# Optimization experiments

Hardware: AMD Instinct MI355X
Metric: run time of the kernel (lower is better)

## Reference

```python
import jax, jax.numpy as jnp
import numpy as np
import math

B, T, E, H, L, V = 256, 256, 64, 8, 6, 65
HS = E // H  # head_size = 8


def _pos_encoding():
    position = jnp.arange(T, dtype=jnp.float32)[:, None]
    div_term = jnp.exp(jnp.arange(0, E, 2, dtype=jnp.float32) * (-(math.log(10000.0) / E)))
    pe = jnp.zeros((T, E), dtype=jnp.float32)
    pe = pe.at[:, 0::2].set(jnp.sin(position * div_term))
    pe = pe.at[:, 1::2].set(jnp.cos(position * div_term))
    return pe


def _layernorm(x, g, b, eps=1e-5):
    mu = jnp.mean(x, axis=-1, keepdims=True)
    var = jnp.var(x, axis=-1, keepdims=True)
    return (x - mu) * jax.lax.rsqrt(var + eps) * g + b


def setup_inputs() -> dict:
    key = jax.random.key(0)
    ks = jax.random.split(key, 20)
    s = 0.02
    return {
        "inputs": jax.random.randint(ks[0], (B, T), 0, V),
        "labels": jax.random.randint(ks[1], (B, T), 0, V),
        "emb": jax.random.normal(ks[2], (V, E), jnp.float32) * s,
        "Wq": jax.random.normal(ks[3], (L, E, E), jnp.float32) * s,
        "bq": jnp.zeros((L, E), jnp.float32),
        "Wk": jax.random.normal(ks[4], (L, E, E), jnp.float32) * s,
        "bk": jnp.zeros((L, E), jnp.float32),
        "Wv": jax.random.normal(ks[5], (L, E, E), jnp.float32) * s,
        "bv": jnp.zeros((L, E), jnp.float32),
        "Wo": jax.random.normal(ks[6], (L, E, E), jnp.float32) * s,
        "bo": jnp.zeros((L, E), jnp.float32),
        "ln1_g": jnp.ones((L, E), jnp.float32),
        "ln1_b": jnp.zeros((L, E), jnp.float32),
        "ln2_g": jnp.ones((L, E), jnp.float32),
        "ln2_b": jnp.zeros((L, E), jnp.float32),
        "W1": jax.random.normal(ks[7], (L, E, 4 * E), jnp.float32) * s,
        "b1": jnp.zeros((L, 4 * E), jnp.float32),
        "W2": jax.random.normal(ks[8], (L, 4 * E, E), jnp.float32) * s,
        "b2": jnp.zeros((L, E), jnp.float32),
        "Wout": jax.random.normal(ks[9], (E, V), jnp.float32) * s,
        "bout": jnp.zeros((V,), jnp.float32),
    }


def reference(inputs, labels, emb, Wq, bq, Wk, bk, Wv, bv, Wo, bo,
              ln1_g, ln1_b, ln2_g, ln2_b, W1, b1, W2, b2, Wout, bout):
    x = emb[inputs] + _pos_encoding()[None, :, :]  # [B,T,E]
    causal = jnp.triu(jnp.ones((T, T), dtype=bool), k=1)  # True above diagonal -> masked
    scale = 1.0 / jnp.sqrt(jnp.float32(HS))
    for l in range(L):
        q = (x @ Wq[l] + bq[l]).reshape(B, T, H, HS)
        k = (x @ Wk[l] + bk[l]).reshape(B, T, H, HS)
        v = (x @ Wv[l] + bv[l]).reshape(B, T, H, HS)
        scores = jnp.einsum('bqhd,bkhd->bhqk', q, k) * scale  # [B,H,T,T]
        scores = jnp.where(causal, jnp.float32(-1e9), scores)
        attn = jax.nn.softmax(scores, axis=-1)
        o = jnp.einsum('bhqk,bkhd->bqhd', attn, v).reshape(B, T, E)
        x = _layernorm(x + (o @ Wo[l] + bo[l]), ln1_g[l], ln1_b[l])
        ff = jax.nn.relu(x @ W1[l] + b1[l]) @ W2[l] + b2[l]
        x = _layernorm(x + ff, ln2_g[l], ln2_b[l])
    logits = (x @ Wout + bout).reshape(B * T, V)
    logp = jax.nn.log_softmax(logits, axis=-1)
    loss = -jnp.mean(jnp.take_along_axis(logp, labels.reshape(B * T, 1), axis=-1))
    return logits, loss
```

## Files before the change

### kernel.cpp

```cpp
#include <hip/hip_runtime.h>
#include <math.h>

#define VOCAB 65
#define NBATCH 256

typedef __attribute__((ext_vector_type(8))) short bf16x8;
typedef __attribute__((ext_vector_type(4))) float f32x4;

#define MFMA16(a, b, c) __builtin_amdgcn_mfma_f32_16x16x32_bf16((a), (b), (c), 0, 0, 0)

__device__ __forceinline__ unsigned short f2b(float f) {
    union { float f; unsigned u; } v; v.f = f;
    unsigned r = (v.u + 0x7fffu + ((v.u >> 16) & 1u)) >> 16;
    return (unsigned short)r;
}
__device__ __forceinline__ unsigned cvtpk(float lo, float hi) {
    unsigned r; asm("v_cvt_pk_bf16_f32 %0, %1, %2" : "=v"(r) : "v"(lo), "v"(hi)); return r;
}
__device__ __forceinline__ unsigned short f2b1(float v) { return (unsigned short)cvtpk(v, v); }
__device__ __forceinline__ float b2f(unsigned short h) {
    union { unsigned u; float f; } v; v.u = ((unsigned)h) << 16; return v.f;
}
__device__ __forceinline__ float lo2f(unsigned wd) {
    union { unsigned u; float f; } v; v.u = wd << 16; return v.f;
}
__device__ __forceinline__ float hi2f(unsigned wd) {
    union { unsigned u; float f; } v; v.u = wd & 0xffff0000u; return v.f;
}

__global__ __launch_bounds__(256)
void prep_kernel(const float* __restrict__ Wq, const float* __restrict__ Wk,
                 const float* __restrict__ Wv, const float* __restrict__ Wo,
                 const float* __restrict__ W1, const float* __restrict__ W2,
                 const float* __restrict__ Wout, unsigned short* __restrict__ wbuf) {
    int l = blockIdx.y;
    int idx = blockIdx.x * 256 + threadIdx.x;
    if (l < 6) {
        float v; unsigned short* dst;
        if (idx < 12288) {
            int mat = idx >> 12, m = (idx >> 6) & 63, k = idx & 63;
            const float* W = mat == 0 ? Wq : (mat == 1 ? Wk : Wv);
            v = W[l * 4096 + k * 64 + m];
            dst = wbuf + l * 12288 + idx;
        } else if (idx < 16384) {
            int j = idx - 12288; int m = j >> 6, k = j & 63;
            v = Wo[l * 4096 + k * 64 + m];
            dst = wbuf + 73728 + l * 4096 + j;
        } else if (idx < 32768) {
            int j = idx - 16384; int m = j >> 6, k = j & 63;
            v = W1[l * 16384 + k * 256 + m];
            dst = wbuf + 98304 + l * 16384 + j;
        } else {
            int j = idx - 32768; int m = j >> 8, k = j & 255;
            v = W2[l * 16384 + k * 64 + m];
            dst = wbuf + 196608 + l * 16384 + j;
        }
        *dst = f2b(v);
    } else {
        if (idx < 5120) {
            int m = idx >> 6, k = idx & 63;
            float v = (m < 65) ? Wout[k * 65 + m] : 0.f;
            wbuf[294912 + idx] = f2b(v);
        } else if (idx < 21504) {
            int j = idx - 5120; int t = j >> 6, e = j & 63;
            int i2 = e >> 1;
            float div = expf(-(float)(2 * i2) * 0.14391156831212788f);
            float ang = (float)t * div;
            ((float*)(wbuf + 300032))[j] = (e & 1) ? cosf(ang) : sinf(ang);
        }
    }
}

__global__ __launch_bounds__(1024)
void tf_kernel(const int* __restrict__ inp, const int* __restrict__ labels,
               const float* __restrict__ emb,
               const float* __restrict__ bq, const float* __restrict__ bk,
               const float* __restrict__ bv, const float* __restrict__ bo,
               const float* __restrict__ ln1g, const float* __restrict__ ln1b,
               const float* __restrict__ ln2g, const float* __restrict__ ln2b,
               const float* __restrict__ b1, const float* __restrict__ b2,
               const float* __restrict__ bout,
               const unsigned short* __restrict__ wbuf,
               float* __restrict__ out_logits, float* __restrict__ partials) {
    __shared__ __attribute__((aligned(16))) char smem[143424];
    unsigned short (*xb)[72]      = (unsigned short (*)[72])(smem);
    unsigned short (*res)[72]     = (unsigned short (*)[72])(smem + 36864);
    unsigned short (*q2)[24]      = (unsigned short (*)[24])(smem + 73728);
    unsigned short (*k2)[24]      = (unsigned short (*)[24])(smem + 86016);
    unsigned short (*vt)[264]     = (unsigned short (*)[264])(smem + 98304);
    unsigned short (*pcb)[16][40] = (unsigned short (*)[16][40])(smem + 106752);
    unsigned short (*proj)[72]    = (unsigned short (*)[72])(smem + 73728);
    unsigned short (*hb)[136]     = (unsigned short (*)[136])(smem + 73728);
    float* red = (float*)(smem + 143360);

    const unsigned short* wqkvt = wbuf;
    const unsigned short* wot   = wbuf + 73728;
    const unsigned short* w1t   = wbuf + 98304;
    const unsigned short* w2t   = wbuf + 196608;
    const unsigned short* woutt = wbuf + 294912;
    const float* pef = (const float*)(wbuf + 300032);

    const int b = blockIdx.x;
    const int tid = threadIdx.x;
    const int w = tid >> 6;
    const int lane = tid & 63;
    const int cc = lane & 15;
    const int gg = lane >> 4;

    const bf16x8 zf = {0, 0, 0, 0, 0, 0, 0, 0};
    const bf16x8 ones = {(short)0x3F80, (short)0x3F80, (short)0x3F80, (short)0x3F80,
                         (short)0x3F80, (short)0x3F80, (short)0x3F80, (short)0x3F80};

    {
        int r = tid >> 2, q = tid & 3;
        int id = inp[b * 256 + r];
        const float4* er = (const float4*)(emb + id * 64 + q * 16);
        const float4* pr = (const float4*)(pef + r * 64 + q * 16);
        unsigned nw[8];
        #pragma unroll
        for (int j = 0; j < 4; ++j) {
            float4 ev = er[j], pv = pr[j];
            nw[2 * j]     = cvtpk(ev.x + pv.x, ev.y + pv.y);
            nw[2 * j + 1] = cvtpk(ev.z + pv.z, ev.w + pv.w);
        }
        *(uint4*)&xb[r][16 * q]      = make_uint4(nw[0], nw[1], nw[2], nw[3]);
        *(uint4*)&xb[r][16 * q + 8]  = make_uint4(nw[4], nw[5], nw[6], nw[7]);
        *(uint4*)&res[r][16 * q]     = make_uint4(nw[0], nw[1], nw[2], nw[3]);
        *(uint4*)&res[r][16 * q + 8] = make_uint4(nw[4], nw[5], nw[6], nw[7]);
    }
    __syncthreads();

    auto ownerLN = [&](const float* gp_, const float* bp_) {
        int row = tid >> 2, q = tid & 3;
        uint4 p0 = *(const uint4*)&proj[row][16 * q];
        uint4 p1 = *(const uint4*)&proj[row][16 * q + 8];
        uint4 r0 = *(const uint4*)&res[row][16 * q];
        uint4 r1 = *(const uint4*)&res[row][16 * q + 8];
        unsigned pw[8] = {p0.x, p0.y, p0.z, p0.w, p1.x, p1.y, p1.z, p1.w};
        unsigned rw[8] = {r0.x, r0.y, r0.z, r0.w, r1.x, r1.y, r1.z, r1.w};
        float xv[16];
        float s = 0.f, s2 = 0.f;
        #pragma unroll
        for (int j = 0; j < 8; ++j) {
            float x0 = lo2f(rw[j]) + lo2f(pw[j]);
            float x1 = hi2f(rw[j]) + hi2f(pw[j]);
            xv[2 * j] = x0; xv[2 * j + 1] = x1;
            s += x0 + x1; s2 += x0 * x0 + x1 * x1;
        }
        s  += __shfl_xor(s, 1, 64);  s  += __shfl_xor(s, 2, 64);
        s2 += __shfl_xor(s2, 1, 64); s2 += __shfl_xor(s2, 2, 64);
        float mu = s * 0.015625f;
        float var = s2 * 0.015625f - mu * mu;
        float rstd = rsqrtf(var + 1e-5f);
        const float4* gp = (const float4*)(gp_ + 16 * q);
        const float4* bp = (const float4*)(bp_ + 16 * q);
        unsigned nw[8];
        #pragma unroll
        for (int j = 0; j < 4; ++j) {
            float4 gv = gp[j], bv2 = bp[j];
            float n0 = (xv[4 * j]     - mu) * rstd * gv.x + bv2.x;
            float n1 = (xv[4 * j + 1] - mu) * rstd * gv.y + bv2.y;
            float n2 = (xv[4 * j + 2] - mu) * rstd * gv.z + bv2.z;
            float n3 = (xv[4 * j + 3] - mu) * rstd * gv.w + bv2.w;
            nw[2 * j]     = cvtpk(n0, n1);
            nw[2 * j + 1] = cvtpk(n2, n3);
        }
        *(uint4*)&res[row][16 * q]     = make_uint4(nw[0], nw[1], nw[2], nw[3]);
        *(uint4*)&res[row][16 * q + 8] = make_uint4(nw[4], nw[5], nw[6], nw[7]);
        *(uint4*)&xb[row][16 * q]      = make_uint4(nw[0], nw[1], nw[2], nw[3]);
        *(uint4*)&xb[row][16 * q + 8]  = make_uint4(nw[4], nw[5], nw[6], nw[7]);
    };

    for (int l = 0; l < 6; ++l) {
        const unsigned short* Wqkv = wqkvt + l * 12288;

        bf16x8 a0 = *(const bf16x8*)&xb[16 * w + cc][8 * gg];
        bf16x8 a1 = *(const bf16x8*)&xb[16 * w + cc][32 + 8 * gg];

        #pragma unroll
        for (int p = 0; p < 4; ++p) {
            __syncthreads();
            #pragma unroll
            for (int mat = 0; mat < 3; ++mat) {
                const unsigned short* Wt = Wqkv + mat * 4096;
                bf16x8 bf0 = *(const bf16x8*)&Wt[(16 * p + cc) * 64 + 8 * gg];
                bf16x8 bf1 = *(const bf16x8*)&Wt[(16 * p + cc) * 64 + 32 + 8 * gg];
                const float* bias = (mat == 0 ? bq : (mat == 1 ? bk : bv)) + l * 64;
                float bb = bias[16 * p + cc];
                f32x4 c = {0.f, 0.f, 0.f, 0.f};
                c = MFMA16(a0, bf0, c);
                c = MFMA16(a1, bf1, c);
                if (mat == 0) {
                    #pragma unroll
                    for (int r = 0; r < 4; ++r)
                        q2[16 * w + 4 * gg + r][cc] = f2b1((c[r] + bb) * 0.35355339059327373f);
                } else if (mat == 1) {
                    #pragma unroll
                    for (int r = 0; r < 4; ++r)
                        k2[16 * w + 4 * gg + r][cc] = f2b1(c[r] + bb);
                } else {
                    uint2 pk;
                    pk.x = cvtpk(c[0] + bb, c[1] + bb);
                    pk.y = cvtpk(c[2] + bb, c[3] + bb);
                    *(uint2*)&vt[cc][16 * w + 4 * gg] = pk;
                }
            }
            __syncthreads();

            #pragma unroll
            for (int hh = 0; hh < 2; ++hh) {
                const int h = 2 * p + hh;
                const int hoff = 8 * hh;
                int i0 = (w + 4 * p) & 15;
                int i = hh ? (15 - i0) : i0;
                bf16x8 qf = zf;
                if (gg == 0) qf = *(const bf16x8*)&q2[16 * i + cc][hoff];
                f32x4 o = {0.f, 0.f, 0.f, 0.f};
                int full = i >> 1;
                for (int jc = 0; jc < full; ++jc) {
                    #pragma unroll
                    for (int jt2 = 0; jt2 < 2; ++jt2) {
                        int jt = 2 * jc + jt2;
                        bf16x8 kf = zf;
                        if (gg == 0) kf = *(const bf16x8*)&k2[16 * jt + cc][hoff];
                        f32x4 sc = {0.f, 0.f, 0.f, 0.f};
                        sc = MFMA16(kf, qf, sc);
                        uint2 pk;
                        pk.x = cvtpk(__expf(sc[0]), __expf(sc[1]));
                        pk.y = cvtpk(__expf(sc[2]), __expf(sc[3]));
                        *(uint2*)&pcb[w][cc][16 * jt2 + 4 * gg] = pk;
                    }
                    asm volatile("" ::: "memory");
                    bf16x8 pa = *(const bf16x8*)&pcb[w][cc][8 * gg];
                    bf16x8 vb;
                    if (cc < 8)       vb = *(const bf16x8*)&vt[hoff + cc][32 * jc + 8 * gg];
                    else if (cc == 8) vb = ones;
                    else              vb = zf;
                    o = MFMA16(pa, vb, o);
                    asm volatile("" ::: "memory");
                }
                {
                    int jc = full;
                    #pragma unroll
                    for (int jt2 = 0; jt2 < 2; ++jt2) {
                        int jt = 2 * jc + jt2;
                        uint2 pk = make_uint2(0u, 0u);
                        if (jt <= i) {
                            bf16x8 kf = zf;
                            if (gg == 0) kf = *(const bf16x8*)&k2[16 * jt + cc][hoff];
                            f32x4 sc = {0.f, 0.f, 0.f, 0.f};
                            sc = MFMA16(kf, qf, sc);
                            float pv[4];
                            #pragma unroll
                            for (int r = 0; r < 4; ++r) {
                                float pp = __expf(sc[r]);
                                if (jt == i && 4 * gg + r > cc) pp = 0.f;
                                pv[r] = pp;
                            }
                            pk.x = cvtpk(pv[0], pv[1]);
                            pk.y = cvtpk(pv[2], pv[3]);
                        }
                        *(uint2*)&pcb[w][cc][16 * jt2 + 4 * gg] = pk;
                    }
                    asm volatile("" ::: "memory");
                    bf16x8 pa = *(const bf16x8*)&pcb[w][cc][8 * gg];
                    bf16x8 vb;
                    if (cc < 8)       vb = *(const bf16x8*)&vt[hoff + cc][32 * jc + 8 * gg];
                    else if (cc == 8) vb = ones;
                    else              vb = zf;
                    o = MFMA16(pa, vb, o);
                    asm volatile("" ::: "memory");
                }
                #pragma unroll
                for (int r = 0; r < 4; ++r) {
                    float rs = __shfl(o[r], (lane & 48) + 8, 64);
                    float ov = o[r] * __builtin_amdgcn_rcpf(rs);
                    if (cc < 8)
                        xb[16 * i + 4 * gg + r][8 * h + cc] = f2b1(ov);
                }
            }
        }
        __syncthreads();

        {
            const unsigned short* Wt = wot + l * 4096;
            int n = w & 3;
            bf16x8 bf0 = *(const bf16x8*)&Wt[(16 * n + cc) * 64 + 8 * gg];
            bf16x8 bf1 = *(const bf16x8*)&Wt[(16 * n + cc) * 64 + 32 + 8 * gg];
            float bb = bo[l * 64 + 16 * n + cc];
            #pragma unroll
            for (int mi = 0; mi < 4; ++mi) {
                int mt = 4 * (w >> 2) + mi;
                bf16x8 o0 = *(const bf16x8*)&xb[16 * mt + cc][8 * gg];
                bf16x8 o1 = *(const bf16x8*)&xb[16 * mt + cc][32 + 8 * gg];
                f32x4 c = {0.f, 0.f, 0.f, 0.f};
                c = MFMA16(o0, bf0, c);
                c = MFMA16(o1, bf1, c);
                #pragma unroll
                for (int r = 0; r < 4; ++r)
                    proj[16 * mt + 4 * gg + r][16 * n + cc] = f2b1(c[r] + bb);
            }
        }
        __syncthreads();
        ownerLN(ln1g + l * 64, ln1b + l * 64);
        __syncthreads();

        f32x4 facc[4];
        #pragma unroll
        for (int t = 0; t < 4; ++t) facc[t] = {0.f, 0.f, 0.f, 0.f};
        #pragma unroll
        for (int ch = 0; ch < 2; ++ch) {
            if (ch) __syncthreads();
            {
                const unsigned short* Wt = w1t + l * 16384;
                int n8 = w & 7, mgrp = w >> 3;
                int gcol = 128 * ch + 16 * n8 + cc;
                bf16x8 bf0 = *(const bf16x8*)&Wt[gcol * 64 + 8 * gg];
                bf16x8 bf1 = *(const bf16x8*)&Wt[gcol * 64 + 32 + 8 * gg];
                float bb = b1[l * 256 + gcol];
                #pragma unroll
                for (int mi = 0; mi < 8; ++mi) {
                    int mt = 8 * mgrp + mi;
                    bf16x8 x0 = *(const bf16x8*)&xb[16 * mt + cc][8 * gg];
                    bf16x8 x1 = *(const bf16x8*)&xb[16 * mt + cc][32 + 8 * gg];
                    f32x4 c = {0.f, 0.f, 0.f, 0.f};
                    c = MFMA16(x0, bf0, c);
                    c = MFMA16(x1, bf1, c);
                    #pragma unroll
                    for (int r = 0; r < 4; ++r)
                        hb[16 * mt + 4 * gg + r][16 * n8 + cc] = f2b1(fmaxf(c[r] + bb, 0.f));
                }
            }
            __syncthreads();
            {
                const unsigned short* Wt = w2t + l * 16384;
                int n = w & 3;
                #pragma unroll
                for (int ks = 0; ks < 4; ++ks) {
                    bf16x8 bf0 = *(const bf16x8*)&Wt[(16 * n + cc) * 256 + 128 * ch + 32 * ks + 8 * gg];
                    #pragma unroll
                    for (int mi = 0; mi < 4; ++mi) {
                        int mt = 4 * (w >> 2) + mi;
                        bf16x8 h0 = *(const bf16x8*)&hb[16 * mt + cc][32 * ks + 8 * gg];
                        facc[mi] = MFMA16(h0, bf0, facc[mi]);
                    }
                }
            }
        }
        __syncthreads();
        {
            int n = w & 3;
            float bb = b2[l * 64 + 16 * n + cc];
            #pragma unroll
            for (int mi = 0; mi < 4; ++mi) {
                int mt = 4 * (w >> 2) + mi;
                #pragma unroll
                for (int r = 0; r < 4; ++r)
                    proj[16 * mt + 4 * gg + r][16 * n + cc] = f2b1(facc[mi][r] + bb);
            }
        }
        __syncthreads();
        ownerLN(ln2g + l * 64, ln2b + l * 64);
        __syncthreads();
    }

    {
        bf16x8 a0 = *(const bf16x8*)&xb[16 * w + cc][8 * gg];
        bf16x8 a1 = *(const bf16x8*)&xb[16 * w + cc][32 + 8 * gg];
        #pragma unroll
        for (int t = 0; t < 5; ++t) {
            bf16x8 bf0 = *(const bf16x8*)&woutt[(16 * t + cc) * 64 + 8 * gg];
            bf16x8 bf1 = *(const bf16x8*)&woutt[(16 * t + cc) * 64 + 32 + 8 * gg];
            f32x4 c = {0.f, 0.f, 0.f, 0.f};
            c = MFMA16(a0, bf0, c);
            c = MFMA16(a1, bf1, c);
            int col = 16 * t + cc;
            if (col < 65) {
                float bb = bout[col];
                #pragma unroll
                for (int r = 0; r < 4; ++r) {
                    int row = 16 * w + 4 * gg + r;
                    float v = c[r] + bb;
                    out_logits[((size_t)b * 256 + row) * 65 + col] = v;
                    proj[row][col] = f2b1(v);
                }
            }
        }
    }
    __syncthreads();

    {
        int r = tid >> 2, q4 = tid & 3;
        float sum = 0.f;
        for (int c2 = q4; c2 < 65; c2 += 4) sum += __expf(b2f(proj[r][c2]));
        sum += __shfl_xor(sum, 1, 64);
        sum += __shfl_xor(sum, 2, 64);
        float nll = 0.f;
        if (q4 == 0) {
            int lab = labels[b * 256 + r];
            nll = logf(sum) - b2f(proj[r][lab]);
        }
        #pragma unroll
        for (int m = 1; m < 64; m <<= 1) nll += __shfl_xor(nll, m, 64);
        if (lane == 0) red[w] = nll;
        __syncthreads();
        if (tid == 0) {
            float s = 0.f;
            #pragma unroll
            for (int i = 0; i < 16; ++i) s += red[i];
            partials[b] = s;
        }
    }
}

__global__ __launch_bounds__(64)
void loss_reduce(const float* __restrict__ partials, float* __restrict__ out) {
    int t = threadIdx.x;
    float s = partials[t] + partials[t + 64] + partials[t + 128] + partials[t + 192];
    #pragma unroll
    for (int m = 1; m < 64; m <<= 1) s += __shfl_xor(s, m, 64);
    if (t == 0) out[0] = s * (1.f / 65536.f);
}

extern "C" void kernel_launch(void* const* d_in, const int* in_sizes, int n_in,
                              void* d_out, int out_size, void* d_ws, size_t ws_size,
                              hipStream_t stream) {
    const int*   inputs = (const int*)d_in[0];
    const int*   labels = (const int*)d_in[1];
    const float* emb  = (const float*)d_in[2];
    const float* Wq   = (const float*)d_in[3];
    const float* bq   = (const float*)d_in[4];
    const float* Wk   = (const float*)d_in[5];
    const float* bk   = (const float*)d_in[6];
    const float* Wv   = (const float*)d_in[7];
    const float* bv   = (const float*)d_in[8];
    const float* Wo   = (const float*)d_in[9];
    const float* bo   = (const float*)d_in[10];
    const float* ln1g = (const float*)d_in[11];
    const float* ln1b = (const float*)d_in[12];
    const float* ln2g = (const float*)d_in[13];
    const float* ln2b = (const float*)d_in[14];
    const float* W1   = (const float*)d_in[15];
    const float* b1   = (const float*)d_in[16];
    const float* W2   = (const float*)d_in[17];
    const float* b2   = (const float*)d_in[18];
    const float* Wout = (const float*)d_in[19];
    const float* bout = (const float*)d_in[20];

    float* logits = (float*)d_out;
    float* loss   = logits + (size_t)65536 * 65;

    float* partials = (float*)d_ws;
    unsigned short* wbuf = (unsigned short*)((char*)d_ws + 1024);

    prep_kernel<<<dim3(192, 7), 256, 0, stream>>>(Wq, Wk, Wv, Wo, W1, W2, Wout, wbuf);
    tf_kernel<<<NBATCH, 1024, 0, stream>>>(inputs, labels, emb,
                                           bq, bk, bv, bo,
                                           ln1g, ln1b, ln2g, ln2b,
                                           b1, b2, bout,
                                           wbuf, logits, partials);
    loss_reduce<<<1, 64, 0, stream>>>(partials, loss);
}
```

Measured before the change: 348.5 us.

## Halve block to 512 threads and keep residual in registers

```diff
diff --git a/kernel.cpp b/kernel.cpp
--- a/kernel.cpp
+++ b/kernel.cpp
@@ -71,7 +71,7 @@
     }
 }
 
-__global__ __launch_bounds__(1024)
+__global__ __launch_bounds__(512)
 void tf_kernel(const int* __restrict__ inp, const int* __restrict__ labels,
                const float* __restrict__ emb,
                const float* __restrict__ bq, const float* __restrict__ bk,
@@ -82,16 +82,15 @@
                const float* __restrict__ bout,
                const unsigned short* __restrict__ wbuf,
                float* __restrict__ out_logits, float* __restrict__ partials) {
-    __shared__ __attribute__((aligned(16))) char smem[143424];
+    __shared__ __attribute__((aligned(16))) char smem[106528];
     unsigned short (*xb)[72]      = (unsigned short (*)[72])(smem);
-    unsigned short (*res)[72]     = (unsigned short (*)[72])(smem + 36864);
-    unsigned short (*q2)[24]      = (unsigned short (*)[24])(smem + 73728);
-    unsigned short (*k2)[24]      = (unsigned short (*)[24])(smem + 86016);
-    unsigned short (*vt)[264]     = (unsigned short (*)[264])(smem + 98304);
-    unsigned short (*pcb)[16][40] = (unsigned short (*)[16][40])(smem + 106752);
-    unsigned short (*proj)[72]    = (unsigned short (*)[72])(smem + 73728);
-    unsigned short (*hb)[136]     = (unsigned short (*)[136])(smem + 73728);
-    float* red = (float*)(smem + 143360);
+    unsigned short (*q2)[24]      = (unsigned short (*)[24])(smem + 36864);
+    unsigned short (*k2)[24]      = (unsigned short (*)[24])(smem + 49152);
+    unsigned short (*vt)[264]     = (unsigned short (*)[264])(smem + 61440);
+    unsigned short (*pcb)[16][40] = (unsigned short (*)[16][40])(smem + 69888);
+    unsigned short (*proj)[72]    = (unsigned short (*)[72])(smem + 36864);
+    unsigned short (*hb)[136]     = (unsigned short (*)[136])(smem + 36864);
+    float* red = (float*)(smem + 106496);
 
     const unsigned short* wqkvt = wbuf;
     const unsigned short* wot   = wbuf + 73728;
@@ -111,71 +110,70 @@
     const bf16x8 ones = {(short)0x3F80, (short)0x3F80, (short)0x3F80, (short)0x3F80,
                          (short)0x3F80, (short)0x3F80, (short)0x3F80, (short)0x3F80};
 
+    unsigned rr[16];
+    const int lrow = tid >> 1, lq = tid & 1;
+
     {
-        int r = tid >> 2, q = tid & 3;
-        int id = inp[b * 256 + r];
-        const float4* er = (const float4*)(emb + id * 64 + q * 16);
-        const float4* pr = (const float4*)(pef + r * 64 + q * 16);
-        unsigned nw[8];
-        #pragma unroll
-        for (int j = 0; j < 4; ++j) {
+        int id = inp[b * 256 + lrow];
+        const float4* er = (const float4*)(emb + id * 64 + 32 * lq);
+        const float4* pr = (const float4*)(pef + lrow * 64 + 32 * lq);
+        #pragma unroll
+        for (int j = 0; j < 8; ++j) {
             float4 ev = er[j], pv = pr[j];
-            nw[2 * j]     = cvtpk(ev.x + pv.x, ev.y + pv.y);
-            nw[2 * j + 1] = cvtpk(ev.z + pv.z, ev.w + pv.w);
-        }
-        *(uint4*)&xb[r][16 * q]      = make_uint4(nw[0], nw[1], nw[2], nw[3]);
-        *(uint4*)&xb[r][16 * q + 8]  = make_uint4(nw[4], nw[5], nw[6], nw[7]);
-        *(uint4*)&res[r][16 * q]     = make_uint4(nw[0], nw[1], nw[2], nw[3]);
-        *(uint4*)&res[r][16 * q + 8] = make_uint4(nw[4], nw[5], nw[6], nw[7]);
+            rr[2 * j]     = cvtpk(ev.x + pv.x, ev.y + pv.y);
+            rr[2 * j + 1] = cvtpk(ev.z + pv.z, ev.w + pv.w);
+        }
+        #pragma unroll
+        for (int j = 0; j < 4; ++j)
+            *(uint4*)&xb[lrow][32 * lq + 8 * j] = make_uint4(rr[4 * j], rr[4 * j + 1], rr[4 * j + 2], rr[4 * j + 3]);
     }
     __syncthreads();
 
     auto ownerLN = [&](const float* gp_, const float* bp_) {
-        int row = tid >> 2, q = tid & 3;
-        uint4 p0 = *(const uint4*)&proj[row][16 * q];
-        uint4 p1 = *(const uint4*)&proj[row][16 * q + 8];
-        uint4 r0 = *(const uint4*)&res[row][16 * q];
-        uint4 r1 = *(const uint4*)&res[row][16 * q + 8];
-        unsigned pw[8] = {p0.x, p0.y, p0.z, p0.w, p1.x, p1.y, p1.z, p1.w};
-        unsigned rw[8] = {r0.x, r0.y, r0.z, r0.w, r1.x, r1.y, r1.z, r1.w};
-        float xv[16];
+        unsigned pw[16];
+        #pragma unroll
+        for (int j = 0; j < 4; ++j) {
+            uint4 p = *(const uint4*)&proj[lrow][32 * lq + 8 * j];
+            pw[4 * j] = p.x; pw[4 * j + 1] = p.y; pw[4 * j + 2] = p.z; pw[4 * j + 3] = p.w;
+        }
+        float xv[32];
         float s = 0.f, s2 = 0.f;
         #pragma unroll
-        for (int j = 0; j < 8; ++j) {
-            float x0 = lo2f(rw[j]) + lo2f(pw[j]);
-            float x1 = hi2f(rw[j]) + hi2f(pw[j]);
+        for (int j = 0; j < 16; ++j) {
+            float x0 = lo2f(rr[j]) + lo2f(pw[j]);
+            float x1 = hi2f(rr[j]) + hi2f(pw[j]);
             xv[2 * j] = x0; xv[2 * j + 1] = x1;
             s += x0 + x1; s2 += x0 * x0 + x1 * x1;
         }
-        s  += __shfl_xor(s, 1, 64);  s  += __shfl_xor(s, 2, 64);
-        s2 += __shfl_xor(s2, 1, 64); s2 += __shfl_xor(s2, 2, 64);
+        s  += __shfl_xor(s, 1, 64);
+        s2 += __shfl_xor(s2, 1, 64);
         float mu = s * 0.015625f;
         float var = s2 * 0.015625f - mu * mu;
         float rstd = rsqrtf(var + 1e-5f);
-        const float4* gp = (const float4*)(gp_ + 16 * q);
-        const float4* bp = (const float4*)(bp_ + 16 * q);
-        unsigned nw[8];
-        #pragma unroll
-        for (int j = 0; j < 4; ++j) {
+        const float4* gp = (const float4*)(gp_ + 32 * lq);
+        const float4* bp = (const float4*)(bp_ + 32 * lq);
+        #pragma unroll
+        for (int j = 0; j < 8; ++j) {
             float4 gv = gp[j], bv2 = bp[j];
             float n0 = (xv[4 * j]     - mu) * rstd * gv.x + bv2.x;
             float n1 = (xv[4 * j + 1] - mu) * rstd * gv.y + bv2.y;
             float n2 = (xv[4 * j + 2] - mu) * rstd * gv.z + bv2.z;
             float n3 = (xv[4 * j + 3] - mu) * rstd * gv.w + bv2.w;
-            nw[2 * j]     = cvtpk(n0, n1);
-            nw[2 * j + 1] = cvtpk(n2, n3);
-        }
-        *(uint4*)&res[row][16 * q]     = make_uint4(nw[0], nw[1], nw[2], nw[3]);
-        *(uint4*)&res[row][16 * q + 8] = make_uint4(nw[4], nw[5], nw[6], nw[7]);
-        *(uint4*)&xb[row][16 * q]      = make_uint4(nw[0], nw[1], nw[2], nw[3]);
-        *(uint4*)&xb[row][16 * q + 8]  = make_uint4(nw[4], nw[5], nw[6], nw[7]);
+            rr[2 * j]     = cvtpk(n0, n1);
+            rr[2 * j + 1] = cvtpk(n2, n3);
+        }
+        #pragma unroll
+        for (int j = 0; j < 4; ++j)
+            *(uint4*)&xb[lrow][32 * lq + 8 * j] = make_uint4(rr[4 * j], rr[4 * j + 1], rr[4 * j + 2], rr[4 * j + 3]);
     };
 
     for (int l = 0; l < 6; ++l) {
         const unsigned short* Wqkv = wqkvt + l * 12288;
 
-        bf16x8 a0 = *(const bf16x8*)&xb[16 * w + cc][8 * gg];
-        bf16x8 a1 = *(const bf16x8*)&xb[16 * w + cc][32 + 8 * gg];
+        bf16x8 af00 = *(const bf16x8*)&xb[16 * (2 * w)     + cc][8 * gg];
+        bf16x8 af01 = *(const bf16x8*)&xb[16 * (2 * w)     + cc][32 + 8 * gg];
+        bf16x8 af10 = *(const bf16x8*)&xb[16 * (2 * w + 1) + cc][8 * gg];
+        bf16x8 af11 = *(const bf16x8*)&xb[16 * (2 * w + 1) + cc][32 + 8 * gg];
 
         #pragma unroll
         for (int p = 0; p < 4; ++p) {
@@ -187,22 +185,26 @@
                 bf16x8 bf1 = *(const bf16x8*)&Wt[(16 * p + cc) * 64 + 32 + 8 * gg];
                 const float* bias = (mat == 0 ? bq : (mat == 1 ? bk : bv)) + l * 64;
                 float bb = bias[16 * p + cc];
-                f32x4 c = {0.f, 0.f, 0.f, 0.f};
-                c = MFMA16(a0, bf0, c);
-                c = MFMA16(a1, bf1, c);
-                if (mat == 0) {
-                    #pragma unroll
-                    for (int r = 0; r < 4; ++r)
-                        q2[16 * w + 4 * gg + r][cc] = f2b1((c[r] + bb) * 0.35355339059327373f);
-                } else if (mat == 1) {
-                    #pragma unroll
-                    for (int r = 0; r < 4; ++r)
-                        k2[16 * w + 4 * gg + r][cc] = f2b1(c[r] + bb);
-                } else {
-                    uint2 pk;
-                    pk.x = cvtpk(c[0] + bb, c[1] + bb);
-                    pk.y = cvtpk(c[2] + bb, c[3] + bb);
-                    *(uint2*)&vt[cc][16 * w + 4 * gg] = pk;
+                #pragma unroll
+                for (int mi = 0; mi < 2; ++mi) {
+                    int mt = 2 * w + mi;
+                    f32x4 c = {0.f, 0.f, 0.f, 0.f};
+                    c = MFMA16(mi ? af10 : af00, bf0, c);
+                    c = MFMA16(mi ? af11 : af01, bf1, c);
+                    if (mat == 0) {
+                        #pragma unroll
+                        for (int r = 0; r < 4; ++r)
+                            q2[16 * mt + 4 * gg + r][cc] = f2b1((c[r] + bb) * 0.35355339059327373f);
+                    } else if (mat == 1) {
+                        #pragma unroll
+                        for (int r = 0; r < 4; ++r)
+                            k2[16 * mt + 4 * gg + r][cc] = f2b1(c[r] + bb);
+                    } else {
+                        uint2 pk;
+                        pk.x = cvtpk(c[0] + bb, c[1] + bb);
+                        pk.y = cvtpk(c[2] + bb, c[3] + bb);
+                        *(uint2*)&vt[cc][16 * mt + 4 * gg] = pk;
+                    }
                 }
             }
             __syncthreads();
@@ -211,72 +213,75 @@
             for (int hh = 0; hh < 2; ++hh) {
                 const int h = 2 * p + hh;
                 const int hoff = 8 * hh;
-                int i0 = (w + 4 * p) & 15;
-                int i = hh ? (15 - i0) : i0;
-                bf16x8 qf = zf;
-                if (gg == 0) qf = *(const bf16x8*)&q2[16 * i + cc][hoff];
-                f32x4 o = {0.f, 0.f, 0.f, 0.f};
-                int full = i >> 1;
-                for (int jc = 0; jc < full; ++jc) {
-                    #pragma unroll
-                    for (int jt2 = 0; jt2 < 2; ++jt2) {
-                        int jt = 2 * jc + jt2;
-                        bf16x8 kf = zf;
-                        if (gg == 0) kf = *(const bf16x8*)&k2[16 * jt + cc][hoff];
-                        f32x4 sc = {0.f, 0.f, 0.f, 0.f};
-                        sc = MFMA16(kf, qf, sc);
-                        uint2 pk;
-                        pk.x = cvtpk(__expf(sc[0]), __expf(sc[1]));
-                        pk.y = cvtpk(__expf(sc[2]), __expf(sc[3]));
-                        *(uint2*)&pcb[w][cc][16 * jt2 + 4 * gg] = pk;
-                    }
-                    asm volatile("" ::: "memory");
-                    bf16x8 pa = *(const bf16x8*)&pcb[w][cc][8 * gg];
-                    bf16x8 vb;
-                    if (cc < 8)       vb = *(const bf16x8*)&vt[hoff + cc][32 * jc + 8 * gg];
-                    else if (cc == 8) vb = ones;
-                    else              vb = zf;
-                    o = MFMA16(pa, vb, o);
-                    asm volatile("" ::: "memory");
-                }
-                {
-                    int jc = full;
-                    #pragma unroll
-                    for (int jt2 = 0; jt2 < 2; ++jt2) {
-                        int jt = 2 * jc + jt2;
-                        uint2 pk = make_uint2(0u, 0u);
-                        if (jt <= i) {
+                int a_ = (w + h) & 7;
+                #pragma unroll
+                for (int s = 0; s < 2; ++s) {
+                    int i = s ? (15 - a_) : a_;
+                    bf16x8 qf = zf;
+                    if (gg == 0) qf = *(const bf16x8*)&q2[16 * i + cc][hoff];
+                    f32x4 o = {0.f, 0.f, 0.f, 0.f};
+                    int full = i >> 1;
+                    for (int jc = 0; jc < full; ++jc) {
+                        #pragma unroll
+                        for (int jt2 = 0; jt2 < 2; ++jt2) {
+                            int jt = 2 * jc + jt2;
                             bf16x8 kf = zf;
                             if (gg == 0) kf = *(const bf16x8*)&k2[16 * jt + cc][hoff];
                             f32x4 sc = {0.f, 0.f, 0.f, 0.f};
                             sc = MFMA16(kf, qf, sc);
-                            float pv[4];
-                            #pragma unroll
-                            for (int r = 0; r < 4; ++r) {
-                                float pp = __expf(sc[r]);
-                                if (jt == i && 4 * gg + r > cc) pp = 0.f;
-                                pv[r] = pp;
+                            uint2 pk;
+                            pk.x = cvtpk(__expf(sc[0]), __expf(sc[1]));
+                            pk.y = cvtpk(__expf(sc[2]), __expf(sc[3]));
+                            *(uint2*)&pcb[w][cc][16 * jt2 + 4 * gg] = pk;
+                        }
+                        asm volatile("" ::: "memory");
+                        bf16x8 pa = *(const bf16x8*)&pcb[w][cc][8 * gg];
+                        bf16x8 vb;
+                        if (cc < 8)       vb = *(const bf16x8*)&vt[hoff + cc][32 * jc + 8 * gg];
+                        else if (cc == 8) vb = ones;
+                        else              vb = zf;
+                        o = MFMA16(pa, vb, o);
+                        asm volatile("" ::: "memory");
+                    }
+                    {
+                        int jc = full;
+                        #pragma unroll
+                        for (int jt2 = 0; jt2 < 2; ++jt2) {
+                            int jt = 2 * jc + jt2;
+                            uint2 pk = make_uint2(0u, 0u);
+                            if (jt <= i) {
+                                bf16x8 kf = zf;
+                                if (gg == 0) kf = *(const bf16x8*)&k2[16 * jt + cc][hoff];
+                                f32x4 sc = {0.f, 0.f, 0.f, 0.f};
+                                sc = MFMA16(kf, qf, sc);
+                                float pv[4];
+                                #pragma unroll
+                                for (int r = 0; r < 4; ++r) {
+                                    float pp = __expf(sc[r]);
+                                    if (jt == i && 4 * gg + r > cc) pp = 0.f;
+                                    pv[r] = pp;
+                                }
+                                pk.x = cvtpk(pv[0], pv[1]);
+                                pk.y = cvtpk(pv[2], pv[3]);
                             }
-                            pk.x = cvtpk(pv[0], pv[1]);
-                            pk.y = cvtpk(pv[2], pv[3]);
+                            *(uint2*)&pcb[w][cc][16 * jt2 + 4 * gg] = pk;
                         }
-                        *(uint2*)&pcb[w][cc][16 * jt2 + 4 * gg] = pk;
+                        asm volatile("" ::: "memory");
+                        bf16x8 pa = *(const bf16x8*)&pcb[w][cc][8 * gg];
+                        bf16x8 vb;
+                        if (cc < 8)       vb = *(const bf16x8*)&vt[hoff + cc][32 * jc + 8 * gg];
+                        else if (cc == 8) vb = ones;
+                        else              vb = zf;
+                        o = MFMA16(pa, vb, o);
+                        asm volatile("" ::: "memory");
                     }
-                    asm volatile("" ::: "memory");
-                    bf16x8 pa = *(const bf16x8*)&pcb[w][cc][8 * gg];
-                    bf16x8 vb;
-                    if (cc < 8)       vb = *(const bf16x8*)&vt[hoff + cc][32 * jc + 8 * gg];
-                    else if (cc == 8) vb = ones;
-                    else              vb = zf;
-                    o = MFMA16(pa, vb, o);
-                    asm volatile("" ::: "memory");
-                }
-                #pragma unroll
-                for (int r = 0; r < 4; ++r) {
-                    float rs = __shfl(o[r], (lane & 48) + 8, 64);
-                    float ov = o[r] * __builtin_amdgcn_rcpf(rs);
-                    if (cc < 8)
-                        xb[16 * i + 4 * gg + r][8 * h + cc] = f2b1(ov);
+                    #pragma unroll
+                    for (int r = 0; r < 4; ++r) {
+                        float rs = __shfl(o[r], (lane & 48) + 8, 64);
+                        float ov = o[r] * __builtin_amdgcn_rcpf(rs);
+                        if (cc < 8)
+                            xb[16 * i + 4 * gg + r][8 * h + cc] = f2b1(ov);
+                    }
                 }
             }
         }
@@ -289,8 +294,8 @@
             bf16x8 bf1 = *(const bf16x8*)&Wt[(16 * n + cc) * 64 + 32 + 8 * gg];
             float bb = bo[l * 64 + 16 * n + cc];
             #pragma unroll
-            for (int mi = 0; mi < 4; ++mi) {
-                int mt = 4 * (w >> 2) + mi;
+            for (int mi = 0; mi < 8; ++mi) {
+                int mt = 8 * (w >> 2) + mi;
                 bf16x8 o0 = *(const bf16x8*)&xb[16 * mt + cc][8 * gg];
                 bf16x8 o1 = *(const bf16x8*)&xb[16 * mt + cc][32 + 8 * gg];
                 f32x4 c = {0.f, 0.f, 0.f, 0.f};
@@ -305,22 +310,20 @@
         ownerLN(ln1g + l * 64, ln1b + l * 64);
         __syncthreads();
 
-        f32x4 facc[4];
-        #pragma unroll
-        for (int t = 0; t < 4; ++t) facc[t] = {0.f, 0.f, 0.f, 0.f};
+        f32x4 facc[8];
+        #pragma unroll
+        for (int t = 0; t < 8; ++t) facc[t] = {0.f, 0.f, 0.f, 0.f};
         #pragma unroll
         for (int ch = 0; ch < 2; ++ch) {
             if (ch) __syncthreads();
             {
                 const unsigned short* Wt = w1t + l * 16384;
-                int n8 = w & 7, mgrp = w >> 3;
-                int gcol = 128 * ch + 16 * n8 + cc;
+                int gcol = 128 * ch + 16 * w + cc;
                 bf16x8 bf0 = *(const bf16x8*)&Wt[gcol * 64 + 8 * gg];
                 bf16x8 bf1 = *(const bf16x8*)&Wt[gcol * 64 + 32 + 8 * gg];
                 float bb = b1[l * 256 + gcol];
                 #pragma unroll
-                for (int mi = 0; mi < 8; ++mi) {
-                    int mt = 8 * mgrp + mi;
+                for (int mt = 0; mt < 16; ++mt) {
                     bf16x8 x0 = *(const bf16x8*)&xb[16 * mt + cc][8 * gg];
                     bf16x8 x1 = *(const bf16x8*)&xb[16 * mt + cc][32 + 8 * gg];
                     f32x4 c = {0.f, 0.f, 0.f, 0.f};
@@ -328,7 +331,7 @@
                     c = MFMA16(x1, bf1, c);
                     #pragma unroll
                     for (int r = 0; r < 4; ++r)
-                        hb[16 * mt + 4 * gg + r][16 * n8 + cc] = f2b1(fmaxf(c[r] + bb, 0.f));
+                        hb[16 * mt + 4 * gg + r][16 * w + cc] = f2b1(fmaxf(c[r] + bb, 0.f));
                 }
             }
             __syncthreads();
@@ -339,8 +342,8 @@
                 for (int ks = 0; ks < 4; ++ks) {
                     bf16x8 bf0 = *(const bf16x8*)&Wt[(16 * n + cc) * 256 + 128 * ch + 32 * ks + 8 * gg];
                     #pragma unroll
-                    for (int mi = 0; mi < 4; ++mi) {
-                        int mt = 4 * (w >> 2) + mi;
+                    for (int mi = 0; mi < 8; ++mi) {
+                        int mt = 8 * (w >> 2) + mi;
                         bf16x8 h0 = *(const bf16x8*)&hb[16 * mt + cc][32 * ks + 8 * gg];
                         facc[mi] = MFMA16(h0, bf0, facc[mi]);
                     }
@@ -352,8 +355,8 @@
             int n = w & 3;
             float bb = b2[l * 64 + 16 * n + cc];
             #pragma unroll
-            for (int mi = 0; mi < 4; ++mi) {
-                int mt = 4 * (w >> 2) + mi;
+            for (int mi = 0; mi < 8; ++mi) {
+                int mt = 8 * (w >> 2) + mi;
                 #pragma unroll
                 for (int r = 0; r < 4; ++r)
                     proj[16 * mt + 4 * gg + r][16 * n + cc] = f2b1(facc[mi][r] + bb);
@@ -364,41 +367,39 @@
         __syncthreads();
     }
 
-    {
-        bf16x8 a0 = *(const bf16x8*)&xb[16 * w + cc][8 * gg];
-        bf16x8 a1 = *(const bf16x8*)&xb[16 * w + cc][32 + 8 * gg];
-        #pragma unroll
-        for (int t = 0; t < 5; ++t) {
-            bf16x8 bf0 = *(const bf16x8*)&woutt[(16 * t + cc) * 64 + 8 * gg];
-            bf16x8 bf1 = *(const bf16x8*)&woutt[(16 * t + cc) * 64 + 32 + 8 * gg];
-            f32x4 c = {0.f, 0.f, 0.f, 0.f};
-            c = MFMA16(a0, bf0, c);
-            c = MFMA16(a1, bf1, c);
-            int col = 16 * t + cc;
-            if (col < 65) {
-                float bb = bout[col];
-                #pragma unroll
-                for (int r = 0; r < 4; ++r) {
-                    int row = 16 * w + 4 * gg + r;
-                    float v = c[r] + bb;
-                    out_logits[((size_t)b * 256 + row) * 65 + col] = v;
-                    proj[row][col] = f2b1(v);
-                }
+    #pragma unroll
+    for (int t = 0; t < 10; ++t) {
+        int id = w + 8 * t;
+        int n = id >> 4, mt = id & 15;
+        bf16x8 a0 = *(const bf16x8*)&xb[16 * mt + cc][8 * gg];
+        bf16x8 a1 = *(const bf16x8*)&xb[16 * mt + cc][32 + 8 * gg];
+        bf16x8 bf0 = *(const bf16x8*)&woutt[(16 * n + cc) * 64 + 8 * gg];
+        bf16x8 bf1 = *(const bf16x8*)&woutt[(16 * n + cc) * 64 + 32 + 8 * gg];
+        f32x4 c = {0.f, 0.f, 0.f, 0.f};
+        c = MFMA16(a0, bf0, c);
+        c = MFMA16(a1, bf1, c);
+        int col = 16 * n + cc;
+        if (col < 65) {
+            float bb = bout[col];
+            #pragma unroll
+            for (int r = 0; r < 4; ++r) {
+                int row = 16 * mt + 4 * gg + r;
+                float v = c[r] + bb;
+                out_logits[((size_t)b * 256 + row) * 65 + col] = v;
+                proj[row][col] = f2b1(v);
             }
         }
     }
     __syncthreads();
 
     {
-        int r = tid >> 2, q4 = tid & 3;
         float sum = 0.f;
-        for (int c2 = q4; c2 < 65; c2 += 4) sum += __expf(b2f(proj[r][c2]));
+        for (int c2 = lq; c2 < 65; c2 += 2) sum += __expf(b2f(proj[lrow][c2]));
         sum += __shfl_xor(sum, 1, 64);
-        sum += __shfl_xor(sum, 2, 64);
         float nll = 0.f;
-        if (q4 == 0) {
-            int lab = labels[b * 256 + r];
-            nll = logf(sum) - b2f(proj[r][lab]);
+        if (lq == 0) {
+            int lab = labels[b * 256 + lrow];
+            nll = logf(sum) - b2f(proj[lrow][lab]);
         }
         #pragma unroll
         for (int m = 1; m < 64; m <<= 1) nll += __shfl_xor(nll, m, 64);
@@ -407,7 +408,7 @@
         if (tid == 0) {
             float s = 0.f;
             #pragma unroll
-            for (int i = 0; i < 16; ++i) s += red[i];
+            for (int i = 0; i < 8; ++i) s += red[i];
             partials[b] = s;
         }
     }
@@ -454,10 +455,10 @@
     unsigned short* wbuf = (unsigned short*)((char*)d_ws + 1024);
 
     prep_kernel<<<dim3(192, 7), 256, 0, stream>>>(Wq, Wk, Wv, Wo, W1, W2, Wout, wbuf);
-    tf_kernel<<<NBATCH, 1024, 0, stream>>>(inputs, labels, emb,
-                                           bq, bk, bv, bo,
-                                           ln1g, ln1b, ln2g, ln2b,
-                                           b1, b2, bout,
-                                           wbuf, logits, partials);
+    tf_kernel<<<NBATCH, 512, 0, stream>>>(inputs, labels, emb,
+                                          bq, bk, bv, bo,
+                                          ln1g, ln1b, ln2g, ln2b,
+                                          b1, b2, bout,
+                                          wbuf, logits, partials);
     loss_reduce<<<1, 64, 0, stream>>>(partials, loss);
 }
```

New measurement: 309.7 us. 1.13x faster.
